# Kernel tuning notes

Measured on AMD Instinct MI355X. Metric: run time of the kernel, lower is better.

The kernel has to match this reference:

```python
import jax, jax.numpy as jnp
import numpy as np

HEADS = 16


def setup_inputs() -> dict:
    key = jax.random.key(0)
    k1, k2, k3 = jax.random.split(key, 3)
    B, N, C = 4, 2048, 1024
    x = jax.random.normal(k1, (B, N, C), dtype=jnp.float32)
    w_qkv = jax.random.normal(k2, (C, 3 * C), dtype=jnp.float32) * (C ** -0.5)
    b_qkv = jnp.zeros((3 * C,), dtype=jnp.float32)
    w_out = jax.random.normal(k3, (C, C), dtype=jnp.float32) * (C ** -0.5)
    b_out = jnp.zeros((C,), dtype=jnp.float32)
    return {"x": x, "w_qkv": w_qkv, "b_qkv": b_qkv, "w_out": w_out, "b_out": b_out}


def reference(x, w_qkv, b_qkv, w_out, b_out):
    # Dropout layers act as identity in eval mode.
    B, N, C = x.shape
    H = HEADS
    Dh = C // H
    scale = Dh ** -0.5
    qkv = x @ w_qkv + b_qkv                        # [B, N, 3C]
    qkv = qkv.reshape(B, N, 3, H, Dh)
    q = qkv[:, :, 0].transpose(0, 2, 1, 3)         # [B, H, N, Dh]
    k = qkv[:, :, 1].transpose(0, 2, 1, 3)
    v = qkv[:, :, 2].transpose(0, 2, 1, 3)
    attn = jnp.einsum('bhnd,bhmd->bhnm', q, k) * scale
    attn = jax.nn.softmax(attn, axis=-1)
    out = jnp.einsum('bhnm,bhmd->bhnd', attn, v)   # [B, H, N, Dh]
    out = out.transpose(0, 2, 1, 3).reshape(B, N, C)
    return out @ w_out + b_out
```

## Files before the change

kernel.cpp:

```cpp
#include <hip/hip_runtime.h>

typedef __attribute__((ext_vector_type(8))) short bf16x8;
typedef __attribute__((ext_vector_type(4))) float f32x4;
typedef __attribute__((ext_vector_type(16))) float f32x16;
typedef __attribute__((ext_vector_type(4))) ushort u16x4;

__device__ __forceinline__ ushort f2bf(float f) {
  union { float f; unsigned u; } v; v.f = f;
  unsigned r = v.u + 0x7fffu + ((v.u >> 16) & 1u);
  return (ushort)(r >> 16);
}

__device__ __forceinline__ float bf2f(ushort u) {
  union { float f; unsigned u; } v; v.u = (unsigned)u << 16;
  return v.f;
}

__device__ __forceinline__ unsigned cvt_pk_bf16(float lo, float hi) {
  unsigned r;
  asm("v_cvt_pk_bf16_f32 %0, %1, %2" : "=v"(r) : "v"(lo), "v"(hi));
  return r;
}

__device__ __forceinline__ void permlane32_swap(unsigned& x, unsigned& y) {
  asm("v_permlane32_swap_b32 %0, %1" : "+v"(x), "+v"(y));
}

__device__ __forceinline__ void gload_lds16(const void* g, void* l) {
  __builtin_amdgcn_global_load_lds(
      (const __attribute__((address_space(1))) void*)g,
      (__attribute__((address_space(3))) void*)l, 16, 0, 0);
}


__global__ void cvt_f32_bf16(const float* __restrict__ s, ushort* __restrict__ d, int n) {
  int i = (blockIdx.x * blockDim.x + threadIdx.x) * 4;
  int stride = gridDim.x * blockDim.x * 4;
  for (; i < n; i += stride) {
    float4 v = *reinterpret_cast<const float4*>(s + i);
    ushort4 o;
    o.x = f2bf(v.x); o.y = f2bf(v.y); o.z = f2bf(v.z); o.w = f2bf(v.w);
    *reinterpret_cast<ushort4*>(d + i) = o;
  }
}

__global__ void transpose_cvt(const float* __restrict__ src, ushort* __restrict__ dst,
                              int R, int C) {
  __shared__ float tile[32][33];
  int c0 = blockIdx.x * 32, r0 = blockIdx.y * 32;
  int tx = threadIdx.x, ty = threadIdx.y;
  #pragma unroll
  for (int i = 0; i < 32; i += 8)
    tile[ty + i][tx] = src[(size_t)(r0 + ty + i) * C + c0 + tx];
  __syncthreads();
  #pragma unroll
  for (int i = 0; i < 32; i += 8)
    dst[(size_t)(c0 + ty + i) * R + r0 + tx] = f2bf(tile[tx][ty + i]);
}


__global__ void gemm_qkv(const ushort* __restrict__ A, const ushort* __restrict__ Bt,
                         const float* __restrict__ bias,
                         ushort* __restrict__ q, ushort* __restrict__ k,
                         ushort* __restrict__ vT) {
  constexpr int K = 1024;
  __shared__ __align__(16) ushort sA[128 * 32];
  __shared__ __align__(16) ushort sB[128 * 32];
  const int tid = threadIdx.x;
  const int lane = tid & 63;
  const int w = tid >> 6;
  const int wr = w >> 1, wc = w & 1;
  const int bm = blockIdx.y * 128;
  const int bn = blockIdx.x * 128;
  f32x4 acc[4][4] = {};
  const int srow = lane >> 2;
  const int skb = (lane & 3) * 8;

  for (int kt = 0; kt < K; kt += 32) {
    #pragma unroll
    for (int i = 0; i < 2; ++i) {
      const int chunk = w * 2 + i;
      const int row = chunk * 16 + srow;
      gload_lds16(A + (size_t)(bm + row) * K + kt + skb, sA + chunk * 512);
      gload_lds16(Bt + (size_t)(bn + row) * K + kt + skb, sB + chunk * 512);
    }
    __syncthreads();
    bf16x8 af[4], bfr[4];
    #pragma unroll
    for (int mi = 0; mi < 4; ++mi)
      af[mi] = *(const bf16x8*)(sA + (wr * 64 + mi * 16 + (lane & 15)) * 32 + (lane >> 4) * 8);
    #pragma unroll
    for (int ni = 0; ni < 4; ++ni)
      bfr[ni] = *(const bf16x8*)(sB + (wc * 64 + ni * 16 + (lane & 15)) * 32 + (lane >> 4) * 8);
    #pragma unroll
    for (int mi = 0; mi < 4; ++mi)
      #pragma unroll
      for (int ni = 0; ni < 4; ++ni)
        acc[mi][ni] = __builtin_amdgcn_mfma_f32_16x16x32_bf16(af[mi], bfr[ni], acc[mi][ni], 0, 0, 0);
    __syncthreads();
  }

  #pragma unroll
  for (int mi = 0; mi < 4; ++mi)
    #pragma unroll
    for (int ni = 0; ni < 4; ++ni) {
      const int col = bn + wc * 64 + ni * 16 + (lane & 15);
      const int t = col >> 10;
      const int h = (col >> 6) & 15;
      const int d = col & 63;
      const float bb = bias[col];
      #pragma unroll
      for (int r = 0; r < 4; ++r) {
        const int row = bm + wr * 64 + mi * 16 + (lane >> 4) * 4 + r;
        const int b_ = row >> 11, n = row & 2047;
        const int bh = b_ * 16 + h;
        const ushort hv = f2bf(acc[mi][ni][r] + bb);
        if (t == 0)      q[((size_t)bh * 2048 + n) * 64 + d] = hv;
        else if (t == 1) k[((size_t)bh * 2048 + n) * 64 + d] = hv;
        else             vT[((size_t)bh * 64 + d) * 2048 + n] = hv;
      }
    }
}


__global__ __launch_bounds__(512, 2) void attn_fwd(const ushort* __restrict__ q,
                                                   const ushort* __restrict__ k,
                                                   const ushort* __restrict__ vT,
                                                   ushort* __restrict__ o) {
  __shared__ __align__(16) ushort sK[2][64 * 64];
  __shared__ __align__(16) ushort sV[2][64 * 64];

  const int tid = threadIdx.x, lane = tid & 63, w = tid >> 6;
  const int id = blockIdx.x;
  const int xcd = id & 7, j = id >> 3;
  const int bh = xcd * 8 + (j & 7);
  const int qx = j >> 3;
  const int qrow0 = qx * 256 + w * 32;

  const ushort* Qb = q + (size_t)bh * 2048 * 64;
  const ushort* Kb = k + (size_t)bh * 2048 * 64;
  const ushort* Vb = vT + (size_t)bh * 64 * 2048;
  const int lq = lane & 31, hi = lane >> 5;

  const int srow = lane >> 3;
  const int ssw = ((lane & 7) ^ srow) * 8;
  const int krow = w * 8 + srow;

  gload_lds16(Kb + (size_t)krow * 64 + ssw, &sK[0][w * 512]);
  gload_lds16(Vb + (size_t)krow * 2048 + 0 + ssw, &sV[0][w * 512]);

  const float qs = 0.125f * 1.44269504f;
  bf16x8 qf[4];
  #pragma unroll
  for (int dk = 0; dk < 4; ++dk) {
    bf16x8 t = *(const bf16x8*)(Qb + (size_t)(qrow0 + lq) * 64 + dk * 16 + hi * 8);
    #pragma unroll
    for (int jj = 0; jj < 8; ++jj)
      t[jj] = (short)f2bf(bf2f((ushort)t[jj]) * qs);
    qf[dk] = t;
  }

  float m_run = -1e30f, l_run = 0.f;
  f32x16 oacc[2] = {};

  for (int t = 0; t < 32; ++t) {
    const int cur = t & 1;
    if (t + 1 < 32) {
      const int kv2 = (t + 1) << 6;
      gload_lds16(Kb + (size_t)(kv2 + krow) * 64 + ssw, &sK[cur ^ 1][w * 512]);
      gload_lds16(Vb + (size_t)krow * 2048 + kv2 + ssw, &sV[cur ^ 1][w * 512]);
      asm volatile("s_waitcnt vmcnt(2)" ::: "memory");
    } else {
      asm volatile("s_waitcnt vmcnt(0)" ::: "memory");
    }
    __builtin_amdgcn_s_barrier();
    __builtin_amdgcn_sched_barrier(0);

    const char* kb_ = (const char*)&sK[cur][0];
    const char* vb_ = (const char*)&sV[cur][0];

    f32x16 S[2] = {};
    __builtin_amdgcn_s_setprio(1);
    #pragma unroll
    for (int kvt = 0; kvt < 2; ++kvt) {
      const int row = kvt * 32 + lq;
      const int rsw = (row & 7) << 4;
      #pragma unroll
      for (int dk = 0; dk < 4; ++dk) {
        bf16x8 kf = *(const bf16x8*)(kb_ + row * 128 + ((dk * 32 + hi * 16) ^ rsw));
        S[kvt] = __builtin_amdgcn_mfma_f32_32x32x16_bf16(kf, qf[dk], S[kvt], 0, 0, 0);
      }
    }
    __builtin_amdgcn_s_setprio(0);

    float mx = S[0][0];
    #pragma unroll
    for (int kvt = 0; kvt < 2; ++kvt)
      #pragma unroll
      for (int r = 0; r < 16; ++r) mx = fmaxf(mx, S[kvt][r]);
    const float rm = fmaxf(mx, __shfl_xor(mx, 32, 64));

    if (!__all(rm <= m_run + 8.f)) {
      const float mnew = fmaxf(m_run, rm);
      const float corr = __builtin_amdgcn_exp2f(m_run - mnew);
      m_run = mnew;
      l_run *= corr;
      float cq[16];
      #pragma unroll
      for (int r = 0; r < 16; ++r)
        cq[r] = __shfl(corr, (r & 3) + 8 * (r >> 2) + 4 * hi, 64);
      #pragma unroll
      for (int dt = 0; dt < 2; ++dt)
        #pragma unroll
        for (int r = 0; r < 16; ++r) oacc[dt][r] *= cq[r];
    }

    float psum = 0.f;
    unsigned pk_[2][8];
    #pragma unroll
    for (int kvt = 0; kvt < 2; ++kvt) {
      float e[16];
      #pragma unroll
      for (int r = 0; r < 16; ++r) {
        e[r] = __builtin_amdgcn_exp2f(S[kvt][r] - m_run);
        psum += e[r];
      }
      #pragma unroll
      for (int g = 0; g < 4; ++g) {
        pk_[kvt][g * 2 + 0] = cvt_pk_bf16(e[4 * g + 0], e[4 * g + 1]);
        pk_[kvt][g * 2 + 1] = cvt_pk_bf16(e[4 * g + 2], e[4 * g + 3]);
      }
    }
    psum += __shfl_xor(psum, 32, 64);
    l_run += psum;

    __builtin_amdgcn_s_setprio(1);
    #pragma unroll
    for (int kvt = 0; kvt < 2; ++kvt)
      #pragma unroll
      for (int cc = 0; cc < 2; ++cc) {
        unsigned x0 = pk_[kvt][4 * cc + 0], x1 = pk_[kvt][4 * cc + 1];
        unsigned y0 = pk_[kvt][4 * cc + 2], y1 = pk_[kvt][4 * cc + 3];
        permlane32_swap(x0, y0);
        permlane32_swap(x1, y1);
        union { unsigned u[4]; bf16x8 v; } A;
        A.u[0] = x0; A.u[1] = x1; A.u[2] = y0; A.u[3] = y1;
        const int cg = kvt * 2 + cc;
        #pragma unroll
        for (int dt = 0; dt < 2; ++dt) {
          const int row = dt * 32 + lq;
          bf16x8 vf = *(const bf16x8*)(vb_ + row * 128 + ((cg * 32 + hi * 16) ^ ((row & 7) << 4)));
          oacc[dt] = __builtin_amdgcn_mfma_f32_32x32x16_bf16(A.v, vf, oacc[dt], 0, 0, 0);
        }
      }
    __builtin_amdgcn_s_setprio(0);
    __builtin_amdgcn_s_barrier();
  }

  const int b_ = bh >> 4, h = bh & 15;
  float lf[16];
  #pragma unroll
  for (int r = 0; r < 16; ++r)
    lf[r] = __builtin_amdgcn_rcpf(__shfl(l_run, (r & 3) + 8 * (r >> 2) + 4 * hi, 64));
  #pragma unroll
  for (int dt = 0; dt < 2; ++dt)
    #pragma unroll
    for (int r = 0; r < 16; ++r) {
      const int n = qrow0 + (r & 3) + 8 * (r >> 2) + 4 * hi;
      o[(((size_t)b_ * 2048 + n) * 16 + h) * 64 + dt * 32 + lq] = f2bf(oacc[dt][r] * lf[r]);
    }
}


__global__ void gemm_out(const ushort* __restrict__ A, const ushort* __restrict__ Bt,
                         const float* __restrict__ bias, float* __restrict__ out) {
  constexpr int K = 1024;
  __shared__ __align__(16) ushort sA[128 * 32];
  __shared__ __align__(16) ushort sB[128 * 32];
  const int tid = threadIdx.x;
  const int lane = tid & 63;
  const int w = tid >> 6;
  const int wr = w >> 1, wc = w & 1;
  const int bm = blockIdx.y * 128;
  const int bn = blockIdx.x * 128;
  f32x4 acc[4][4] = {};
  const int srow = lane >> 2;
  const int skb = (lane & 3) * 8;

  for (int kt = 0; kt < K; kt += 32) {
    #pragma unroll
    for (int i = 0; i < 2; ++i) {
      const int chunk = w * 2 + i;
      const int row = chunk * 16 + srow;
      gload_lds16(A + (size_t)(bm + row) * K + kt + skb, sA + chunk * 512);
      gload_lds16(Bt + (size_t)(bn + row) * K + kt + skb, sB + chunk * 512);
    }
    __syncthreads();
    bf16x8 af[4], bfr[4];
    #pragma unroll
    for (int mi = 0; mi < 4; ++mi)
      af[mi] = *(const bf16x8*)(sA + (wr * 64 + mi * 16 + (lane & 15)) * 32 + (lane >> 4) * 8);
    #pragma unroll
    for (int ni = 0; ni < 4; ++ni)
      bfr[ni] = *(const bf16x8*)(sB + (wc * 64 + ni * 16 + (lane & 15)) * 32 + (lane >> 4) * 8);
    #pragma unroll
    for (int mi = 0; mi < 4; ++mi)
      #pragma unroll
      for (int ni = 0; ni < 4; ++ni)
        acc[mi][ni] = __builtin_amdgcn_mfma_f32_16x16x32_bf16(af[mi], bfr[ni], acc[mi][ni], 0, 0, 0);
    __syncthreads();
  }

  #pragma unroll
  for (int mi = 0; mi < 4; ++mi)
    #pragma unroll
    for (int ni = 0; ni < 4; ++ni) {
      const int col = bn + wc * 64 + ni * 16 + (lane & 15);
      const float bb = bias[col];
      #pragma unroll
      for (int r = 0; r < 4; ++r) {
        const int row = bm + wr * 64 + mi * 16 + (lane >> 4) * 4 + r;
        out[(size_t)row * 1024 + col] = acc[mi][ni][r] + bb;
      }
    }
}


extern "C" void kernel_launch(void* const* d_in, const int* in_sizes, int n_in,
                              void* d_out, int out_size, void* d_ws, size_t ws_size,
                              hipStream_t stream) {
  const float* x = (const float*)d_in[0];
  const float* w_qkv = (const float*)d_in[1];
  const float* b_qkv = (const float*)d_in[2];
  const float* w_out = (const float*)d_in[3];
  const float* b_out = (const float*)d_in[4];
  float* out = (float*)d_out;
  char* ws = (char*)d_ws;

  ushort* xb    = (ushort*)(ws);
  ushort* wqkvT = (ushort*)(ws + 16777216);
  ushort* woutT = (ushort*)(ws + 23068672);
  ushort* qb    = (ushort*)(ws + 25165824);
  ushort* kb    = (ushort*)(ws + 41943040);
  ushort* vTb   = (ushort*)(ws + 58720256);
  ushort* attnb = (ushort*)(ws + 75497472);

  cvt_f32_bf16<<<2048, 256, 0, stream>>>(x, xb, 8192 * 1024);
  transpose_cvt<<<dim3(96, 32), dim3(32, 8), 0, stream>>>(w_qkv, wqkvT, 1024, 3072);
  transpose_cvt<<<dim3(32, 32), dim3(32, 8), 0, stream>>>(w_out, woutT, 1024, 1024);
  gemm_qkv<<<dim3(24, 64), 256, 0, stream>>>(xb, wqkvT, b_qkv, qb, kb, vTb);
  attn_fwd<<<512, 512, 0, stream>>>(qb, kb, vTb, attnb);
  gemm_out<<<dim3(8, 64), 256, 0, stream>>>(attnb, woutT, b_out, out);
}
```

Before: 217.3 us.

## Rewrite QKV GEMM with 256x256 tiles, double-buffered LDS and phased MFMA

The QKV projection GEMM moves from 128x128 tiles with a K-step of 32 and single-buffered LDS to 256x256 tiles with a K-step of 64, 512 threads and double-buffered swizzled LDS. Global-to-LDS loads for the next tiles are issued in halves between four MFMA phases, each fenced by barriers and raised priority. This is meant to overlap memory traffic with compute, raise arithmetic intensity and avoid LDS bank conflicts. In exchange it uses more LDS and registers, relies on hand-counted vmcnt waits, and leaves fewer blocks (384) to fill the device.

```diff
diff --git a/kernel.cpp b/kernel.cpp
--- a/kernel.cpp
+++ b/kernel.cpp
@@ -3,7 +3,6 @@
 typedef __attribute__((ext_vector_type(8))) short bf16x8;
 typedef __attribute__((ext_vector_type(4))) float f32x4;
 typedef __attribute__((ext_vector_type(16))) float f32x16;
-typedef __attribute__((ext_vector_type(4))) ushort u16x4;
 
 __device__ __forceinline__ ushort f2bf(float f) {
   union { float f; unsigned u; } v; v.f = f;
@@ -59,67 +58,130 @@
 }
 
 
-__global__ void gemm_qkv(const ushort* __restrict__ A, const ushort* __restrict__ Bt,
-                         const float* __restrict__ bias,
-                         ushort* __restrict__ q, ushort* __restrict__ k,
-                         ushort* __restrict__ vT) {
-  constexpr int K = 1024;
-  __shared__ __align__(16) ushort sA[128 * 32];
-  __shared__ __align__(16) ushort sB[128 * 32];
-  const int tid = threadIdx.x;
-  const int lane = tid & 63;
-  const int w = tid >> 6;
-  const int wr = w >> 1, wc = w & 1;
-  const int bm = blockIdx.y * 128;
-  const int bn = blockIdx.x * 128;
-  f32x4 acc[4][4] = {};
-  const int srow = lane >> 2;
-  const int skb = (lane & 3) * 8;
-
-  for (int kt = 0; kt < K; kt += 32) {
-    #pragma unroll
-    for (int i = 0; i < 2; ++i) {
-      const int chunk = w * 2 + i;
-      const int row = chunk * 16 + srow;
-      gload_lds16(A + (size_t)(bm + row) * K + kt + skb, sA + chunk * 512);
-      gload_lds16(Bt + (size_t)(bn + row) * K + kt + skb, sB + chunk * 512);
-    }
-    __syncthreads();
-    bf16x8 af[4], bfr[4];
+#define STAGE_HALF(dstbuf, srcp, base, t, half)                                    \
+  {                                                                                \
+    _Pragma("unroll")                                                              \
+    for (int l_ = 0; l_ < 2; ++l_) {                                               \
+      const int r_ = (half) * 128 + l_ * 64 + sr;                                  \
+      gload_lds16(srcp + (size_t)((base) + r_) * 1024 + (t) * 64 + scg,            \
+                  (char*)&dstbuf[(t) & 1][0] + (half) * 16384 + l_ * 8192 + tid * 16); \
+    }                                                                              \
+  }
+
+#define LDA8(mh)                                                                   \
+  {                                                                                \
+    _Pragma("unroll")                                                              \
+    for (int mi = 0; mi < 4; ++mi) {                                               \
+      const int row_ = wm * 128 + (mh) * 64 + mi * 16 + lr;                        \
+      const char* p_ = (const char*)&sA[cur][0] + row_ * 128;                      \
+      const int sw_ = (row_ & 7) << 4;                                             \
+      af[mi * 2 + 0] = *(const bf16x8*)(p_ + ((lg * 16) ^ sw_));                   \
+      af[mi * 2 + 1] = *(const bf16x8*)(p_ + ((64 + lg * 16) ^ sw_));              \
+    }                                                                              \
+  }
+
+#define LDB4(nh)                                                                   \
+  {                                                                                \
+    _Pragma("unroll")                                                              \
+    for (int ni = 0; ni < 2; ++ni) {                                               \
+      const int row_ = wn * 64 + (nh) * 32 + ni * 16 + lr;                         \
+      const char* p_ = (const char*)&sB[cur][0] + row_ * 128;                      \
+      const int sw_ = (row_ & 7) << 4;                                             \
+      bf[ni * 2 + 0] = *(const bf16x8*)(p_ + ((lg * 16) ^ sw_));                   \
+      bf[ni * 2 + 1] = *(const bf16x8*)(p_ + ((64 + lg * 16) ^ sw_));              \
+    }                                                                              \
+  }
+
+#define MMQ(mh, nh)                                                                \
+  {                                                                                \
+    _Pragma("unroll")                                                              \
+    for (int kk = 0; kk < 2; ++kk)                                                 \
+      _Pragma("unroll")                                                            \
+      for (int mi = 0; mi < 4; ++mi)                                               \
+        _Pragma("unroll")                                                          \
+        for (int ni = 0; ni < 2; ++ni)                                             \
+          acc[mh][mi][nh][ni] = __builtin_amdgcn_mfma_f32_16x16x32_bf16(           \
+              af[mi * 2 + kk], bf[ni * 2 + kk], acc[mh][mi][nh][ni], 0, 0, 0);     \
+  }
+
+#define PH_SYNC_MFMA(mh, nh)                                                       \
+  __builtin_amdgcn_s_barrier();                                                    \
+  asm volatile("s_waitcnt lgkmcnt(0)" ::: "memory");                               \
+  __builtin_amdgcn_sched_barrier(0);                                               \
+  __builtin_amdgcn_s_setprio(1);                                                   \
+  MMQ(mh, nh);                                                                     \
+  __builtin_amdgcn_s_setprio(0);                                                   \
+  __builtin_amdgcn_s_barrier();
+
+__global__ __launch_bounds__(512, 2) void gemm_qkv(const ushort* __restrict__ A,
+                                                   const ushort* __restrict__ Bt,
+                                                   const float* __restrict__ bias,
+                                                   ushort* __restrict__ q,
+                                                   ushort* __restrict__ k,
+                                                   ushort* __restrict__ vT) {
+  __shared__ __align__(16) ushort sA[2][256 * 64];
+  __shared__ __align__(16) ushort sB[2][256 * 64];
+  const int tid = threadIdx.x, lane = tid & 63, w = tid >> 6;
+  const int wm = w >> 2, wn = w & 3;
+  const int bm = blockIdx.y * 256, bn = blockIdx.x * 256;
+  const int lr = lane & 15, lg = lane >> 4;
+  const int sr = tid >> 3;
+  const int scg = ((tid & 7) ^ (sr & 7)) * 8;
+
+  f32x4 acc[2][4][2][2] = {};
+  bf16x8 af[8], bf[4];
+
+  STAGE_HALF(sA, A, bm, 0, 0);
+  STAGE_HALF(sB, Bt, bn, 0, 1);
+  STAGE_HALF(sA, A, bm, 0, 1);
+  STAGE_HALF(sB, Bt, bn, 0, 0);
+  STAGE_HALF(sA, A, bm, 1, 0);
+  STAGE_HALF(sB, Bt, bn, 1, 1);
+  asm volatile("s_waitcnt vmcnt(4)" ::: "memory");
+  __builtin_amdgcn_s_barrier();
+
+  for (int T = 0; T < 16; ++T) {
+    const int cur = T & 1;
+    LDA8(0); LDB4(0);
+    if (T + 1 < 16) STAGE_HALF(sA, A, bm, T + 1, 1);
+    PH_SYNC_MFMA(0, 0);
+    LDB4(1);
+    if (T + 1 < 16) STAGE_HALF(sB, Bt, bn, T + 1, 0);
+    PH_SYNC_MFMA(0, 1);
+    LDA8(1);
+    if (T + 2 < 16) STAGE_HALF(sA, A, bm, T + 2, 0);
+    PH_SYNC_MFMA(1, 1);
+    LDB4(0);
+    if (T + 2 < 16) STAGE_HALF(sB, Bt, bn, T + 2, 1);
+    if (T < 14) { asm volatile("s_waitcnt vmcnt(4)" ::: "memory"); }
+    else        { asm volatile("s_waitcnt vmcnt(0)" ::: "memory"); }
+    PH_SYNC_MFMA(1, 0);
+  }
+
+  #pragma unroll
+  for (int mh = 0; mh < 2; ++mh)
     #pragma unroll
     for (int mi = 0; mi < 4; ++mi)
-      af[mi] = *(const bf16x8*)(sA + (wr * 64 + mi * 16 + (lane & 15)) * 32 + (lane >> 4) * 8);
-    #pragma unroll
-    for (int ni = 0; ni < 4; ++ni)
-      bfr[ni] = *(const bf16x8*)(sB + (wc * 64 + ni * 16 + (lane & 15)) * 32 + (lane >> 4) * 8);
-    #pragma unroll
-    for (int mi = 0; mi < 4; ++mi)
-      #pragma unroll
-      for (int ni = 0; ni < 4; ++ni)
-        acc[mi][ni] = __builtin_amdgcn_mfma_f32_16x16x32_bf16(af[mi], bfr[ni], acc[mi][ni], 0, 0, 0);
-    __syncthreads();
-  }
-
-  #pragma unroll
-  for (int mi = 0; mi < 4; ++mi)
-    #pragma unroll
-    for (int ni = 0; ni < 4; ++ni) {
-      const int col = bn + wc * 64 + ni * 16 + (lane & 15);
-      const int t = col >> 10;
-      const int h = (col >> 6) & 15;
-      const int d = col & 63;
-      const float bb = bias[col];
-      #pragma unroll
-      for (int r = 0; r < 4; ++r) {
-        const int row = bm + wr * 64 + mi * 16 + (lane >> 4) * 4 + r;
-        const int b_ = row >> 11, n = row & 2047;
-        const int bh = b_ * 16 + h;
-        const ushort hv = f2bf(acc[mi][ni][r] + bb);
-        if (t == 0)      q[((size_t)bh * 2048 + n) * 64 + d] = hv;
-        else if (t == 1) k[((size_t)bh * 2048 + n) * 64 + d] = hv;
-        else             vT[((size_t)bh * 64 + d) * 2048 + n] = hv;
-      }
-    }
+      #pragma unroll
+      for (int nh = 0; nh < 2; ++nh)
+        #pragma unroll
+        for (int ni = 0; ni < 2; ++ni) {
+          const int col = bn + wn * 64 + nh * 32 + ni * 16 + lr;
+          const int t = col >> 10;
+          const int h = (col >> 6) & 15;
+          const int d = col & 63;
+          const float bb = bias[col];
+          #pragma unroll
+          for (int rr = 0; rr < 4; ++rr) {
+            const int row = bm + wm * 128 + mh * 64 + mi * 16 + lg * 4 + rr;
+            const int b_ = row >> 11, n = row & 2047;
+            const int bh = b_ * 16 + h;
+            const ushort hv = f2bf(acc[mh][mi][nh][ni][rr] + bb);
+            if (t == 0)      q[((size_t)bh * 2048 + n) * 64 + d] = hv;
+            else if (t == 1) k[((size_t)bh * 2048 + n) * 64 + d] = hv;
+            else             vT[((size_t)bh * 64 + d) * 2048 + n] = hv;
+          }
+        }
 }
 
 
@@ -243,14 +305,14 @@
         unsigned y0 = pk_[kvt][4 * cc + 2], y1 = pk_[kvt][4 * cc + 3];
         permlane32_swap(x0, y0);
         permlane32_swap(x1, y1);
-        union { unsigned u[4]; bf16x8 v; } A;
-        A.u[0] = x0; A.u[1] = x1; A.u[2] = y0; A.u[3] = y1;
+        union { unsigned u[4]; bf16x8 v; } Am;
+        Am.u[0] = x0; Am.u[1] = x1; Am.u[2] = y0; Am.u[3] = y1;
         const int cg = kvt * 2 + cc;
         #pragma unroll
         for (int dt = 0; dt < 2; ++dt) {
           const int row = dt * 32 + lq;
           bf16x8 vf = *(const bf16x8*)(vb_ + row * 128 + ((cg * 32 + hi * 16) ^ ((row & 7) << 4)));
-          oacc[dt] = __builtin_amdgcn_mfma_f32_32x32x16_bf16(A.v, vf, oacc[dt], 0, 0, 0);
+          oacc[dt] = __builtin_amdgcn_mfma_f32_32x32x16_bf16(Am.v, vf, oacc[dt], 0, 0, 0);
         }
       }
     __builtin_amdgcn_s_setprio(0);
@@ -348,7 +410,7 @@
   cvt_f32_bf16<<<2048, 256, 0, stream>>>(x, xb, 8192 * 1024);
   transpose_cvt<<<dim3(96, 32), dim3(32, 8), 0, stream>>>(w_qkv, wqkvT, 1024, 3072);
   transpose_cvt<<<dim3(32, 32), dim3(32, 8), 0, stream>>>(w_out, woutT, 1024, 1024);
-  gemm_qkv<<<dim3(24, 64), 256, 0, stream>>>(xb, wqkvT, b_qkv, qb, kb, vTb);
+  gemm_qkv<<<dim3(12, 32), 512, 0, stream>>>(xb, wqkvT, b_qkv, qb, kb, vTb);
   attn_fwd<<<512, 512, 0, stream>>>(qb, kb, vTb, attnb);
   gemm_out<<<dim3(8, 64), 256, 0, stream>>>(attnb, woutT, b_out, out);
 }
```

Result: no change. 220.6 us (+1.5%).
